# Optimization experiments

Hardware: AMD Instinct MI355X
Metric: run time of the kernel (lower is better)

The kernel has to match this reference:

```python
import jax, jax.numpy as jnp
import numpy as np

N = 100000   # total nodes
E = 500000   # directed edges
G = 100      # graphs in batch (1000 nodes each)
D = 146      # in/hidden/out dim
C = 10       # classes
BN_EPS = 1e-5


def setup_inputs():
    key = jax.random.key(0)
    ks = jax.random.split(key, 20)
    nodes_feat = jax.random.normal(ks[0], (N, D), jnp.float32)
    src = jax.random.randint(ks[1], (E,), 0, N, dtype=jnp.int32)
    dst = jax.random.randint(ks[2], (E,), 0, N, dtype=jnp.int32)
    graph_ids = (jnp.arange(N, dtype=jnp.int32) // (N // G)).astype(jnp.int32)
    snorm = jnp.full((N,), 1.0 / np.sqrt(N // G), jnp.float32)
    s = 0.05
    W_emb = jax.random.normal(ks[3], (D, D), jnp.float32) * s
    b_emb = jnp.zeros((D,), jnp.float32)
    Ws = jax.random.normal(ks[4], (4, D, D), jnp.float32) * s
    bs = jnp.zeros((4, D), jnp.float32)
    gammas = jnp.ones((4, D), jnp.float32)
    betas = jnp.zeros((4, D), jnp.float32)
    W1 = jax.random.normal(ks[5], (D, D // 2), jnp.float32) * s
    b1 = jnp.zeros((D // 2,), jnp.float32)
    W2 = jax.random.normal(ks[6], (D // 2, D // 4), jnp.float32) * s
    b2 = jnp.zeros((D // 4,), jnp.float32)
    W3 = jax.random.normal(ks[7], (D // 4, C), jnp.float32) * s
    b3 = jnp.zeros((C,), jnp.float32)
    return dict(nodes_feat=nodes_feat, snorm=snorm, W_emb=W_emb, b_emb=b_emb,
                Ws=Ws, bs=bs, gammas=gammas, betas=betas,
                W1=W1, b1=b1, W2=W2, b2=b2, W3=W3, b3=b3,
                src=src, dst=dst, graph_ids=graph_ids)


def _gcn_layer(h, W, b, gamma, beta, src, dst, norm_out, norm_in, snorm):
    h_in = h
    # GraphConv norm='both': D_out^{-1/2} on source, sum-aggregate, D_in^{-1/2} on dest
    m = (h * norm_out[:, None])[src]                     # [E, D] gather
    agg = jax.ops.segment_sum(m, dst, num_segments=N)    # [N, D] scatter-add
    h = agg * norm_in[:, None] @ W + b                   # linear
    h = h * snorm[:, None]                               # graph norm
    mu = jnp.mean(h, axis=0)
    var = jnp.var(h, axis=0)
    h = (h - mu) * jax.lax.rsqrt(var + BN_EPS) * gamma + beta  # batch norm
    h = jax.nn.relu(h)
    return h_in + h                                      # residual


def reference(nodes_feat, snorm, W_emb, b_emb, Ws, bs, gammas, betas,
              W1, b1, W2, b2, W3, b3, src, dst, graph_ids):
    ones_e = jnp.ones((E,), jnp.float32)
    deg_out = jnp.clip(jax.ops.segment_sum(ones_e, src, num_segments=N), 1.0)
    deg_in = jnp.clip(jax.ops.segment_sum(ones_e, dst, num_segments=N), 1.0)
    norm_out = jax.lax.rsqrt(deg_out)
    norm_in = jax.lax.rsqrt(deg_in)

    h = nodes_feat @ W_emb + b_emb                       # embedding_h
    for i in range(4):
        h = _gcn_layer(h, Ws[i], bs[i], gammas[i], betas[i],
                       src, dst, norm_out, norm_in, snorm)

    # mean_nodes per graph
    cnt = jax.ops.segment_sum(jnp.ones((N,), jnp.float32), graph_ids, num_segments=G)
    hg = jax.ops.segment_sum(h, graph_ids, num_segments=G) / cnt[:, None]

    # MLPReadout: 146 -> 73 -> 36 -> 10
    x = jax.nn.relu(hg @ W1 + b1)
    x = jax.nn.relu(x @ W2 + b2)
    return x @ W3 + b3
```

## Files before the change

kernel.cpp:

```cpp
#include <hip/hip_runtime.h>

#define N_NODES 100000
#define N_EDGES 500000
#define N_GRAPHS 100
#define DIM 146
#define APAD 160
#define HPAD 160
#define TPW 160
#define BN_EPS 1e-5f
#define GS_PART 8
#define GS_STRIDE 147
#define ST_PART 4

typedef __bf16 bf16x8 __attribute__((ext_vector_type(8)));
typedef float floatx4 __attribute__((ext_vector_type(4)));
typedef unsigned short ushort_t;
typedef unsigned int uint_t;

__device__ inline ushort_t f2bf(float x) {
  uint_t u = __float_as_uint(x);
  uint_t r = (u + 0x7fffu + ((u >> 16) & 1u)) >> 16;
  return (ushort_t)r;
}
__device__ inline float bf2f(ushort_t b) { return __uint_as_float((uint_t)b << 16); }
__device__ inline uint_t pack2bf(float a, float b) {
  return (uint_t)f2bf(a) | ((uint_t)f2bf(b) << 16);
}
__device__ inline float bflo(uint_t u) { return __uint_as_float(u << 16); }
__device__ inline float bfhi(uint_t u) { return __uint_as_float(u & 0xffff0000u); }

__device__ inline void async_cp16(const ushort_t* g, ushort_t* l) {
  __builtin_amdgcn_global_load_lds((const __attribute__((address_space(1))) void*)g,
                                   (__attribute__((address_space(3))) void*)l, 16, 0, 0);
}

__global__ void hist_kernel(const int* __restrict__ src, const int* __restrict__ dst,
                            int* __restrict__ deg_out, int* __restrict__ deg_in) {
  int e = blockIdx.x * 256 + threadIdx.x;
  if (e < N_EDGES) {
    atomicAdd(&deg_out[src[e]], 1);
    atomicAdd(&deg_in[dst[e]], 1);
  }
}

__global__ void norm_kernel(const int* __restrict__ deg_out, const int* __restrict__ deg_in,
                            float* __restrict__ norm_out, float* __restrict__ norm_in) {
  int v = blockIdx.x * 256 + threadIdx.x;
  if (v < N_NODES) {
    norm_out[v] = rsqrtf((float)max(deg_out[v], 1));
    norm_in[v]  = rsqrtf((float)max(deg_in[v], 1));
  }
}

__global__ void scan1_kernel(const int* __restrict__ deg_in, int* __restrict__ bsums) {
  __shared__ int sred[256];
  int t0 = blockIdx.x * 1024 + threadIdx.x * 4;
  int s = 0;
#pragma unroll
  for (int i = 0; i < 4; i++) { int v = t0 + i; s += (v < N_NODES) ? deg_in[v] : 0; }
  sred[threadIdx.x] = s; __syncthreads();
  for (int off = 128; off > 0; off >>= 1) {
    if (threadIdx.x < off) sred[threadIdx.x] += sred[threadIdx.x + off];
    __syncthreads();
  }
  if (threadIdx.x == 0) bsums[blockIdx.x] = sred[0];
}

__global__ void scan2_kernel(const int* __restrict__ bsums, int* __restrict__ bofs,
                             int* __restrict__ row_ptr, int nb) {
  if (threadIdx.x == 0 && blockIdx.x == 0) {
    int run = 0;
    for (int i = 0; i < nb; i++) { bofs[i] = run; run += bsums[i]; }
    row_ptr[N_NODES] = run;
  }
}

__global__ void scan3_kernel(const int* __restrict__ deg_in, const int* __restrict__ bofs,
                             int* __restrict__ row_ptr) {
  __shared__ int ssc[256];
  int t0 = blockIdx.x * 1024 + threadIdx.x * 4;
  int v4[4]; int s = 0;
#pragma unroll
  for (int i = 0; i < 4; i++) { int v = t0 + i; v4[i] = (v < N_NODES) ? deg_in[v] : 0; s += v4[i]; }
  ssc[threadIdx.x] = s; __syncthreads();
  for (int off = 1; off < 256; off <<= 1) {
    int t = (threadIdx.x >= off) ? ssc[threadIdx.x - off] : 0;
    __syncthreads();
    ssc[threadIdx.x] += t;
    __syncthreads();
  }
  int ex = ssc[threadIdx.x] - s + bofs[blockIdx.x];
#pragma unroll
  for (int i = 0; i < 4; i++) {
    int v = t0 + i;
    if (v < N_NODES) { row_ptr[v] = ex; ex += v4[i]; }
  }
}

__global__ void csr_fill_kernel(const int* __restrict__ src, const int* __restrict__ dst,
                                const int* __restrict__ row_ptr, int* __restrict__ fill,
                                int* __restrict__ csr) {
  int e = blockIdx.x * 256 + threadIdx.x;
  if (e < N_EDGES) {
    int d = dst[e];
    int slot = atomicAdd(&fill[d], 1);
    csr[row_ptr[d] + slot] = src[e];
  }
}

__global__ void wtrans_kernel(const float* __restrict__ W_emb, const float* __restrict__ Ws,
                              ushort_t* __restrict__ Wb, ushort_t* __restrict__ Wh) {
  int idx = blockIdx.x * 256 + threadIdx.x;
  if (idx >= 5 * 5 * 10 * 64 * 8) return;
  int j = idx & 7;
  int t = idx >> 3;
  int lane = t & 63; t >>= 6;
  int nt = t % 10; t /= 10;
  int kc = t % 5;
  int m = t / 5;
  const float* W = (m == 0) ? W_emb : Ws + (size_t)(m - 1) * DIM * DIM;
  int k = kc * 32 + (lane >> 4) * 8 + j;
  int n = nt * 16 + (lane & 15);
  float w = (k < DIM && n < DIM) ? W[k * DIM + n] : 0.f;
  ushort_t hi = f2bf(w);
  float lo = w - bf2f(hi);
  size_t base = (size_t)((((m * 5 + kc) * 10 + nt) * 2) * 64 + lane) * 8 + j;
  Wb[base] = hi;
  Wb[base + 512] = f2bf(lo);
  Wh[(size_t)(((m * 5 + kc) * 10 + nt) * 64 + lane) * 8 + j] = hi;
}

__device__ inline bf16x8 make_frag(const float* __restrict__ nf, int row, int kc, int quad) {
  union { bf16x8 v; ushort_t u[8]; } r;
  const float* p = nf + (size_t)row * DIM + kc * 32 + quad * 8;
  int c0 = kc * 32 + quad * 8;
  if (c0 + 8 <= DIM) {
    float2 q0 = *(const float2*)(p);
    float2 q1 = *(const float2*)(p + 2);
    float2 q2 = *(const float2*)(p + 4);
    float2 q3 = *(const float2*)(p + 6);
    r.u[0] = f2bf(q0.x); r.u[1] = f2bf(q0.y); r.u[2] = f2bf(q1.x); r.u[3] = f2bf(q1.y);
    r.u[4] = f2bf(q2.x); r.u[5] = f2bf(q2.y); r.u[6] = f2bf(q3.x); r.u[7] = f2bf(q3.y);
  } else {
#pragma unroll
    for (int j = 0; j < 8; j++) r.u[j] = (c0 + j < DIM) ? f2bf(p[j]) : (ushort_t)0;
  }
  return r.v;
}

__global__ __launch_bounds__(256, 3) void gemm_embed_kernel(
    const float* __restrict__ nf, const ushort_t* __restrict__ Wb,
    const float* __restrict__ bias, const float* __restrict__ norm_out,
    float* __restrict__ h, ushort_t* __restrict__ hb) {
  __shared__ __align__(16) ushort_t sB[2][10240];
  int wave = threadIdx.x >> 6, lane = threadIdx.x & 63;
  int quad = lane >> 4, l16 = lane & 15;
  int m0 = blockIdx.x * 128 + wave * 32;
  int ra = min(m0 + l16, N_NODES - 1);
  int rb = min(m0 + 16 + l16, N_NODES - 1);

  auto stage = [&](int buf, int kc) {
    const ushort_t* wsrc = Wb + (size_t)kc * 10240 + threadIdx.x * 8;
    ushort_t* ldst = &sB[buf][threadIdx.x * 8];
#pragma unroll
    for (int p = 0; p < 5; p++) async_cp16(wsrc + p * 2048, ldst + p * 2048);
  };

  stage(0, 0);
  __syncthreads();

  floatx4 acc[2][10];
#pragma unroll
  for (int s = 0; s < 2; s++)
#pragma unroll
    for (int nt = 0; nt < 10; nt++) acc[s][nt] = (floatx4){0.f, 0.f, 0.f, 0.f};

#pragma unroll
  for (int kc = 0; kc < 5; kc++) {
    int buf = kc & 1;
    if (kc < 4) stage(buf ^ 1, kc + 1);
    bf16x8 a0 = make_frag(nf, ra, kc, quad);
    bf16x8 a1 = make_frag(nf, rb, kc, quad);
    const ushort_t* bp = &sB[buf][lane * 8];
#pragma unroll
    for (int nt = 0; nt < 10; nt++) {
      bf16x8 bh = *(const bf16x8*)(bp + (nt * 2) * 512);
      bf16x8 bl = *(const bf16x8*)(bp + (nt * 2 + 1) * 512);
      acc[0][nt] = __builtin_amdgcn_mfma_f32_16x16x32_bf16(a0, bh, acc[0][nt], 0, 0, 0);
      acc[1][nt] = __builtin_amdgcn_mfma_f32_16x16x32_bf16(a1, bh, acc[1][nt], 0, 0, 0);
      acc[0][nt] = __builtin_amdgcn_mfma_f32_16x16x32_bf16(a0, bl, acc[0][nt], 0, 0, 0);
      acc[1][nt] = __builtin_amdgcn_mfma_f32_16x16x32_bf16(a1, bl, acc[1][nt], 0, 0, 0);
    }
    __syncthreads();
  }

  float no[2][4];
#pragma unroll
  for (int s = 0; s < 2; s++)
#pragma unroll
    for (int r = 0; r < 4; r++) no[s][r] = norm_out[min(m0 + s * 16 + quad * 4 + r, N_NODES - 1)];

  float* sF = (float*)&sB[0][0];
#pragma unroll
  for (int nt = 0; nt < 5; nt++) {
    int c = nt * 16 + l16;
    float b = bias[c];
#pragma unroll
    for (int s = 0; s < 2; s++)
#pragma unroll
      for (int r = 0; r < 4; r++)
        sF[(wave * 32 + s * 16 + quad * 4 + r) * 80 + c] = acc[s][nt][r] + b;
  }
  __syncthreads();
#pragma unroll
  for (int i = 0; i < 10; i++) {
    int n = threadIdx.x + i * 256;
    int row = n / 20, ch = n - row * 20;
    int grow = blockIdx.x * 128 + row;
    if (grow < N_NODES)
      *((uint4*)(h + (size_t)grow * HPAD) + ch) = ((const uint4*)(sF + row * 80))[ch];
  }
  __syncthreads();
#pragma unroll
  for (int nt = 5; nt < 10; nt++) {
    int c = nt * 16 + l16;
    float b = (c < DIM) ? bias[c] : 0.f;
#pragma unroll
    for (int s = 0; s < 2; s++)
#pragma unroll
      for (int r = 0; r < 4; r++)
        sF[(wave * 32 + s * 16 + quad * 4 + r) * 80 + (c - 80)] = acc[s][nt][r] + b;
  }
  __syncthreads();
#pragma unroll
  for (int i = 0; i < 10; i++) {
    int n = threadIdx.x + i * 256;
    int row = n / 20, ch = n - row * 20;
    int grow = blockIdx.x * 128 + row;
    if (grow < N_NODES)
      *((uint4*)(h + (size_t)grow * HPAD + 80) + ch) = ((const uint4*)(sF + row * 80))[ch];
  }
  __syncthreads();
  ushort_t* sC = &sB[0][0];
#pragma unroll
  for (int nt = 0; nt < 10; nt++) {
    int c = nt * 16 + l16;
    float b = (c < DIM) ? bias[c] : 0.f;
#pragma unroll
    for (int s = 0; s < 2; s++)
#pragma unroll
      for (int r = 0; r < 4; r++)
        sC[(wave * 32 + s * 16 + quad * 4 + r) * 160 + c] = f2bf((acc[s][nt][r] + b) * no[s][r]);
  }
  __syncthreads();
#pragma unroll
  for (int i = 0; i < 10; i++) {
    int n = threadIdx.x + i * 256;
    int row = n / 20, ch = n - row * 20;
    int grow = blockIdx.x * 128 + row;
    if (grow < N_NODES)
      *((uint4*)(hb + (size_t)grow * APAD) + ch) = ((const uint4*)(sC + row * 160))[ch];
  }
}

__global__ __launch_bounds__(256, 4) void gemm_kernel(
    const ushort_t* __restrict__ Abf, const ushort_t* __restrict__ Wh,
    const float* __restrict__ bias, const float* __restrict__ snorm,
    ushort_t* __restrict__ tmpb, float* __restrict__ stats) {
  __shared__ __align__(16) ushort_t sB[2][5120];
  __shared__ float sred[2 * DIM];
  int wave = threadIdx.x >> 6, lane = threadIdx.x & 63;
  int quad = lane >> 4, l16 = lane & 15;
  int m0 = blockIdx.x * 128 + wave * 32;
  int ra = min(m0 + l16, N_NODES - 1);
  int rb = min(m0 + 16 + l16, N_NODES - 1);
  const ushort_t* ap0 = Abf + (size_t)ra * APAD + quad * 8;
  const ushort_t* ap1 = Abf + (size_t)rb * APAD + quad * 8;

  auto stage = [&](int buf, int kc) {
    const ushort_t* wsrc = Wh + (size_t)kc * 5120;
    ushort_t* ldst = &sB[buf][0];
    async_cp16(wsrc + threadIdx.x * 8, ldst + threadIdx.x * 8);
    async_cp16(wsrc + (threadIdx.x + 256) * 8, ldst + (threadIdx.x + 256) * 8);
    if (threadIdx.x < 128)
      async_cp16(wsrc + (threadIdx.x + 512) * 8, ldst + (threadIdx.x + 512) * 8);
  };

  stage(0, 0);
  bf16x8 a0[5], a1[5];
#pragma unroll
  for (int kc = 0; kc < 5; kc++) {
    a0[kc] = *(const bf16x8*)(ap0 + kc * 32);
    a1[kc] = *(const bf16x8*)(ap1 + kc * 32);
  }
  for (int i = threadIdx.x; i < 2 * DIM; i += 256) sred[i] = 0.f;
  __syncthreads();

  floatx4 acc[2][10];
#pragma unroll
  for (int s = 0; s < 2; s++)
#pragma unroll
    for (int nt = 0; nt < 10; nt++) acc[s][nt] = (floatx4){0.f, 0.f, 0.f, 0.f};

  for (int kc = 0; kc < 5; kc++) {
    int buf = kc & 1;
    if (kc < 4) stage(buf ^ 1, kc + 1);
    const ushort_t* bp = &sB[buf][lane * 8];
#pragma unroll
    for (int nt = 0; nt < 10; nt++) {
      bf16x8 bh = *(const bf16x8*)(bp + nt * 512);
      acc[0][nt] = __builtin_amdgcn_mfma_f32_16x16x32_bf16(a0[kc], bh, acc[0][nt], 0, 0, 0);
      acc[1][nt] = __builtin_amdgcn_mfma_f32_16x16x32_bf16(a1[kc], bh, acc[1][nt], 0, 0, 0);
    }
    __syncthreads();
  }

  float sn[2][4];
#pragma unroll
  for (int s = 0; s < 2; s++)
#pragma unroll
    for (int r = 0; r < 4; r++) sn[s][r] = snorm[min(m0 + s * 16 + quad * 4 + r, N_NODES - 1)];
#pragma unroll
  for (int nt = 0; nt < 10; nt++) {
    int c = nt * 16 + l16;
    if (c < DIM) {
      float b = bias[c];
      float ssum = 0.f, ssq = 0.f;
#pragma unroll
      for (int s = 0; s < 2; s++)
#pragma unroll
        for (int r = 0; r < 4; r++) {
          if (m0 + s * 16 + quad * 4 + r < N_NODES) {
            float val = (acc[s][nt][r] + b) * sn[s][r];
            ssum += val; ssq += val * val;
          }
        }
      ssum += __shfl_xor(ssum, 16, 64); ssum += __shfl_xor(ssum, 32, 64);
      ssq  += __shfl_xor(ssq, 16, 64);  ssq  += __shfl_xor(ssq, 32, 64);
      if (quad == 0) {
        atomicAdd(&sred[c], ssum);
        atomicAdd(&sred[DIM + c], ssq);
      }
    }
  }

  ushort_t* sC = &sB[0][0];
#pragma unroll
  for (int half = 0; half < 2; half++) {
    __syncthreads();
    if ((wave >> 1) == half) {
      int lrow = (wave & 1) * 32;
#pragma unroll
      for (int nt = 0; nt < 10; nt++) {
        int c = nt * 16 + l16;
        float b = (c < DIM) ? bias[c] : 0.f;
#pragma unroll
        for (int s = 0; s < 2; s++)
#pragma unroll
          for (int r = 0; r < 4; r++)
            sC[(lrow + s * 16 + quad * 4 + r) * TPW + c] = f2bf((acc[s][nt][r] + b) * sn[s][r]);
      }
    }
    __syncthreads();
    uint4* gp = (uint4*)(tmpb + ((size_t)blockIdx.x * 128 + half * 64) * TPW);
#pragma unroll
    for (int i = 0; i < 5; i++) {
      int n = threadIdx.x + i * 256;
      gp[n] = *(const uint4*)(sC + n * 8);
    }
  }
  float* stp = stats + (blockIdx.x & (ST_PART - 1)) * 2 * DIM;
  for (int i = threadIdx.x; i < 2 * DIM; i += 256) atomicAdd(&stp[i], sred[i]);
}

__global__ __launch_bounds__(256) void agg_kernel(
    const ushort_t* __restrict__ hb, const int* __restrict__ row_ptr,
    const int* __restrict__ csr, const float* __restrict__ norm_in,
    ushort_t* __restrict__ xb) {
  int wid = threadIdx.x >> 6, lane = threadIdx.x & 63;
  int v = blockIdx.x * 4 + wid;
  if (v >= N_NODES) return;
  int e0 = row_ptr[v], e1 = row_ptr[v + 1];
  bool act = lane < 40;
  int col8 = lane * 4;
  float a0 = 0.f, a1 = 0.f, a2 = 0.f, a3 = 0.f;
  float b0 = 0.f, b1 = 0.f, b2 = 0.f, b3 = 0.f;
  int e = e0;
  for (; e + 1 < e1; e += 2) {
    int s0 = csr[e], s1 = csr[e + 1];
    if (act) {
      uint2 u0 = *(const uint2*)(hb + (size_t)s0 * APAD + col8);
      uint2 u1 = *(const uint2*)(hb + (size_t)s1 * APAD + col8);
      a0 += bflo(u0.x); a1 += bfhi(u0.x); a2 += bflo(u0.y); a3 += bfhi(u0.y);
      b0 += bflo(u1.x); b1 += bfhi(u1.x); b2 += bflo(u1.y); b3 += bfhi(u1.y);
    }
  }
  if (e < e1) {
    int s0 = csr[e];
    if (act) {
      uint2 u0 = *(const uint2*)(hb + (size_t)s0 * APAD + col8);
      a0 += bflo(u0.x); a1 += bfhi(u0.x); a2 += bflo(u0.y); a3 += bfhi(u0.y);
    }
  }
  if (act) {
    float ni = norm_in[v];
    uint2 o;
    o.x = pack2bf((a0 + b0) * ni, (a1 + b1) * ni);
    o.y = pack2bf((a2 + b2) * ni, (a3 + b3) * ni);
    *(uint2*)((uint_t*)(xb + (size_t)v * APAD) + lane * 2) = o;
  }
}

__global__ __launch_bounds__(256) void bn_kernel(const ushort_t* __restrict__ tmpb,
                                                 const float* __restrict__ stats,
                                                 const float* __restrict__ gamma,
                                                 const float* __restrict__ beta,
                                                 const float* __restrict__ norm_out,
                                                 float* __restrict__ h,
                                                 ushort_t* __restrict__ hb) {
  __shared__ float2 scs[DIM / 2], shs[DIM / 2];
  int t = threadIdx.x;
  if (t < DIM / 2) {
    int c0 = 2 * t, c1 = c0 + 1;
    float su0 = 0.f, su1 = 0.f, sq0 = 0.f, sq1 = 0.f;
#pragma unroll
    for (int p = 0; p < ST_PART; p++) {
      const float* sp = stats + p * 2 * DIM;
      su0 += sp[c0]; su1 += sp[c1];
      sq0 += sp[DIM + c0]; sq1 += sp[DIM + c1];
    }
    float mu0 = su0 * (1.f / N_NODES), mu1 = su1 * (1.f / N_NODES);
    float v0 = sq0 * (1.f / N_NODES) - mu0 * mu0;
    float v1 = sq1 * (1.f / N_NODES) - mu1 * mu1;
    float s0 = gamma[c0] * rsqrtf(v0 + BN_EPS), s1 = gamma[c1] * rsqrtf(v1 + BN_EPS);
    scs[t] = make_float2(s0, s1);
    shs[t] = make_float2(beta[c0] - mu0 * s0, beta[c1] - mu1 * s1);
  }
  __syncthreads();
  int idx = blockIdx.x * 256 + t;
  if (idx >= N_NODES * (DIM / 2)) return;
  int v = idx / (DIM / 2), c2 = idx - v * (DIM / 2);
  uint_t tu = ((const uint_t*)tmpb)[(size_t)v * (TPW / 2) + c2];
  float2 sc = scs[c2], sh = shs[c2];
  float2* hp = (float2*)(h + (size_t)v * HPAD + 2 * c2);
  float2 hv = *hp;
  float x0 = fmaf(bflo(tu), sc.x, sh.x); x0 = fmaxf(x0, 0.f);
  float x1 = fmaf(bfhi(tu), sc.y, sh.y); x1 = fmaxf(x1, 0.f);
  hv.x += x0; hv.y += x1;
  *hp = hv;
  float no = norm_out[v];
  ((uint_t*)hb)[(size_t)v * (APAD / 2) + c2] = pack2bf(hv.x * no, hv.y * no);
}

__global__ __launch_bounds__(192) void gsum_kernel(
    const ushort_t* __restrict__ tmpb, const float* __restrict__ stats,
    const float* __restrict__ gamma, const float* __restrict__ beta,
    const float* __restrict__ h, const int* __restrict__ gids,
    float* __restrict__ hgp) {
  int t = threadIdx.x;
  if (t > DIM) return;
  float sc = 0.f, sh = 0.f;
  if (t < DIM) {
    float su = 0.f, sq = 0.f;
#pragma unroll
    for (int p = 0; p < ST_PART; p++) {
      const float* sp = stats + p * 2 * DIM;
      su += sp[t]; sq += sp[DIM + t];
    }
    float mu = su * (1.f / N_NODES);
    float var = sq * (1.f / N_NODES) - mu * mu;
    sc = gamma[t] * rsqrtf(var + BN_EPS);
    sh = beta[t] - mu * sc;
  }
  int r0 = blockIdx.x * 64;
  int part = blockIdx.x & (GS_PART - 1);
  float accv = 0.f;
  int g_prev = gids[r0];
  for (int rr = 0; rr < 64; rr++) {
    int r = r0 + rr;
    if (r >= N_NODES) break;
    int g = gids[r];
    if (g != g_prev) {
      atomicAdd(&hgp[(size_t)(part * N_GRAPHS + g_prev) * GS_STRIDE + t], accv);
      accv = 0.f; g_prev = g;
    }
    float val;
    if (t < DIM) {
      float x = fmaf(bf2f(tmpb[(size_t)r * TPW + t]), sc, sh);
      x = fmaxf(x, 0.f);
      val = h[(size_t)r * HPAD + t] + x;
    } else {
      val = 1.f;
    }
    accv += val;
  }
  atomicAdd(&hgp[(size_t)(part * N_GRAPHS + g_prev) * GS_STRIDE + t], accv);
}

__global__ __launch_bounds__(256) void mlp_kernel(
    const float* __restrict__ hgp,
    const float* __restrict__ W1, const float* __restrict__ b1,
    const float* __restrict__ W2, const float* __restrict__ b2,
    const float* __restrict__ W3, const float* __restrict__ b3,
    float* __restrict__ out) {
  __shared__ float hrow[DIM];
  __shared__ float x1[73];
  __shared__ float x2[36];
  int g = blockIdx.x;
  int t = threadIdx.x;
  if (t < DIM) {
    float s = 0.f, cnt = 0.f;
#pragma unroll
    for (int p = 0; p < GS_PART; p++) {
      const float* row = hgp + (size_t)(p * N_GRAPHS + g) * GS_STRIDE;
      s += row[t];
      cnt += row[DIM];
    }
    hrow[t] = s / cnt;
  }
  __syncthreads();
  if (t < 73) {
    float s = b1[t];
    for (int k = 0; k < DIM; k++) s = fmaf(hrow[k], W1[k * 73 + t], s);
    x1[t] = s > 0.f ? s : 0.f;
  }
  __syncthreads();
  if (t < 36) {
    float s = b2[t];
    for (int k = 0; k < 73; k++) s = fmaf(x1[k], W2[k * 36 + t], s);
    x2[t] = s > 0.f ? s : 0.f;
  }
  __syncthreads();
  if (t < 10) {
    float s = b3[t];
    for (int k = 0; k < 36; k++) s = fmaf(x2[k], W3[k * 10 + t], s);
    out[g * 10 + t] = s;
  }
}

extern "C" void kernel_launch(void* const* d_in, const int* in_sizes, int n_in,
                              void* d_out, int out_size, void* d_ws, size_t ws_size,
                              hipStream_t stream) {
  const float* nodes_feat = (const float*)d_in[0];
  const float* snorm  = (const float*)d_in[1];
  const float* W_emb  = (const float*)d_in[2];
  const float* b_emb  = (const float*)d_in[3];
  const float* Ws     = (const float*)d_in[4];
  const float* bs     = (const float*)d_in[5];
  const float* gammas = (const float*)d_in[6];
  const float* betas  = (const float*)d_in[7];
  const float* W1 = (const float*)d_in[8];
  const float* b1 = (const float*)d_in[9];
  const float* W2 = (const float*)d_in[10];
  const float* b2 = (const float*)d_in[11];
  const float* W3 = (const float*)d_in[12];
  const float* b3 = (const float*)d_in[13];
  const int* src  = (const int*)d_in[14];
  const int* dst  = (const int*)d_in[15];
  const int* gids = (const int*)d_in[16];
  float* out = (float*)d_out;

  const int GB = (N_NODES + 127) / 128;
  const int NPADROWS = GB * 128;

  char* base = (char*)d_ws;
  size_t off = 0;
  auto alloc = [&](size_t bytes) { void* p = base + off; off += (bytes + 255) & ~size_t(255); return p; };
  float* h    = (float*)alloc((size_t)N_NODES * HPAD * 4);
  ushort_t* tmpb = (ushort_t*)alloc((size_t)NPADROWS * TPW * 2);
  ushort_t* xb = (ushort_t*)alloc((size_t)N_NODES * APAD * 2);
  ushort_t* hb = (ushort_t*)alloc((size_t)N_NODES * APAD * 2);
  char* zstart = base + off;
  int* deg_out = (int*)alloc(N_NODES * 4);
  int* deg_in  = (int*)alloc(N_NODES * 4);
  int* fill    = (int*)alloc(N_NODES * 4);
  float* stats = (float*)alloc(4 * ST_PART * 2 * DIM * 4);
  float* hgp   = (float*)alloc((size_t)GS_PART * N_GRAPHS * GS_STRIDE * 4);
  size_t zbytes = (size_t)((base + off) - zstart);
  int* row_ptr = (int*)alloc((N_NODES + 1) * 4);
  float* norm_out = (float*)alloc(N_NODES * 4);
  float* norm_in  = (float*)alloc(N_NODES * 4);
  int* csr   = (int*)alloc((size_t)N_EDGES * 4);
  int* bsums = (int*)alloc(128 * 4);
  int* bofs  = (int*)alloc(128 * 4);
  ushort_t* Wb = (ushort_t*)alloc((size_t)5 * 5 * 10 * 2 * 64 * 8 * 2);
  ushort_t* Wh = (ushort_t*)alloc((size_t)5 * 5 * 10 * 64 * 8 * 2);

  hipMemsetAsync(zstart, 0, zbytes, stream);

  hist_kernel<<<(N_EDGES + 255) / 256, 256, 0, stream>>>(src, dst, deg_out, deg_in);
  norm_kernel<<<(N_NODES + 255) / 256, 256, 0, stream>>>(deg_out, deg_in, norm_out, norm_in);
  int nb = (N_NODES + 1023) / 1024;
  scan1_kernel<<<nb, 256, 0, stream>>>(deg_in, bsums);
  scan2_kernel<<<1, 64, 0, stream>>>(bsums, bofs, row_ptr, nb);
  scan3_kernel<<<nb, 256, 0, stream>>>(deg_in, bofs, row_ptr);
  csr_fill_kernel<<<(N_EDGES + 255) / 256, 256, 0, stream>>>(src, dst, row_ptr, fill, csr);
  wtrans_kernel<<<(5 * 5 * 10 * 64 * 8 + 255) / 256, 256, 0, stream>>>(W_emb, Ws, Wb, Wh);

  const size_t WM = (size_t)5 * 10 * 2 * 64 * 8;
  const size_t WHM = (size_t)5 * 10 * 64 * 8;

  gemm_embed_kernel<<<GB, 256, 0, stream>>>(nodes_feat, Wb, b_emb, norm_out, h, hb);

  for (int l = 0; l < 4; l++) {
    float* st = stats + (size_t)l * ST_PART * 2 * DIM;
    agg_kernel<<<(N_NODES + 3) / 4, 256, 0, stream>>>(hb, row_ptr, csr, norm_in, xb);
    gemm_kernel<<<GB, 256, 0, stream>>>(xb, Wh + (size_t)(l + 1) * WHM, bs + l * DIM,
                                        snorm, tmpb, st);
    if (l < 3) {
      bn_kernel<<<(N_NODES * (DIM / 2) + 255) / 256, 256, 0, stream>>>(
          tmpb, st, gammas + l * DIM, betas + l * DIM, norm_out, h, hb);
    } else {
      gsum_kernel<<<(N_NODES + 63) / 64, 192, 0, stream>>>(
          tmpb, st, gammas + l * DIM, betas + l * DIM, h, gids, hgp);
    }
  }

  mlp_kernel<<<N_GRAPHS, 256, 0, stream>>>(hgp, W1, b1, W2, b2, W3, b3, out);
}
```

Measured before the change: 717.7 us.

## Fuse GEMM with batch-norm epilogue via in-kernel grid barrier

```diff
diff --git a/kernel.cpp b/kernel.cpp
--- a/kernel.cpp
+++ b/kernel.cpp
@@ -6,11 +6,11 @@
 #define DIM 146
 #define APAD 160
 #define HPAD 160
-#define TPW 160
 #define BN_EPS 1e-5f
 #define GS_PART 8
 #define GS_STRIDE 147
 #define ST_PART 4
+#define GRID_GB 782
 
 typedef __bf16 bf16x8 __attribute__((ext_vector_type(8)));
 typedef float floatx4 __attribute__((ext_vector_type(4)));
@@ -263,12 +263,18 @@
   }
 }
 
-__global__ __launch_bounds__(256, 4) void gemm_kernel(
+template <bool LAST>
+__global__ __launch_bounds__(256, 4) void gemm_bn_kernel(
     const ushort_t* __restrict__ Abf, const ushort_t* __restrict__ Wh,
     const float* __restrict__ bias, const float* __restrict__ snorm,
-    ushort_t* __restrict__ tmpb, float* __restrict__ stats) {
+    float* __restrict__ stats, const float* __restrict__ gamma,
+    const float* __restrict__ beta, const float* __restrict__ norm_out,
+    float* __restrict__ h, ushort_t* __restrict__ hb,
+    const int* __restrict__ gids, float* __restrict__ hgp, int* __restrict__ gbar) {
   __shared__ __align__(16) ushort_t sB[2][5120];
+  __shared__ __align__(16) ushort_t sHB[5120];
   __shared__ float sred[2 * DIM];
+  __shared__ float sbn[2 * DIM];
   int wave = threadIdx.x >> 6, lane = threadIdx.x & 63;
   int quad = lane >> 4, l16 = lane & 15;
   int m0 = blockIdx.x * 128 + wave * 32;
@@ -315,23 +321,33 @@
     __syncthreads();
   }
 
-  float sn[2][4];
+  float sn[2][4], no[2][4];
 #pragma unroll
   for (int s = 0; s < 2; s++)
 #pragma unroll
-    for (int r = 0; r < 4; r++) sn[s][r] = snorm[min(m0 + s * 16 + quad * 4 + r, N_NODES - 1)];
+    for (int r = 0; r < 4; r++) {
+      int row = min(m0 + s * 16 + quad * 4 + r, N_NODES - 1);
+      sn[s][r] = snorm[row];
+      no[s][r] = LAST ? 0.f : norm_out[row];
+    }
+  float bv[10];
+#pragma unroll
+  for (int nt = 0; nt < 10; nt++) {
+    int c = nt * 16 + l16;
+    bv[nt] = (c < DIM) ? bias[c] : 0.f;
+  }
+
 #pragma unroll
   for (int nt = 0; nt < 10; nt++) {
     int c = nt * 16 + l16;
     if (c < DIM) {
-      float b = bias[c];
       float ssum = 0.f, ssq = 0.f;
 #pragma unroll
       for (int s = 0; s < 2; s++)
 #pragma unroll
         for (int r = 0; r < 4; r++) {
           if (m0 + s * 16 + quad * 4 + r < N_NODES) {
-            float val = (acc[s][nt][r] + b) * sn[s][r];
+            float val = (acc[s][nt][r] + bv[nt]) * sn[s][r];
             ssum += val; ssq += val * val;
           }
         }
@@ -343,34 +359,103 @@
       }
     }
   }
-
-  ushort_t* sC = &sB[0][0];
-#pragma unroll
-  for (int half = 0; half < 2; half++) {
-    __syncthreads();
-    if ((wave >> 1) == half) {
-      int lrow = (wave & 1) * 32;
+  __syncthreads();
+  {
+    float* stp = stats + (blockIdx.x & (ST_PART - 1)) * 2 * DIM;
+    for (int i = threadIdx.x; i < 2 * DIM; i += 256) atomicAdd(&stp[i], sred[i]);
+  }
+
+  __syncthreads();
+  if (threadIdx.x == 0) {
+    __threadfence();
+    atomicAdd(gbar, 1);
+    while (__hip_atomic_load(gbar, __ATOMIC_ACQUIRE, __HIP_MEMORY_SCOPE_AGENT) < GRID_GB)
+      __builtin_amdgcn_s_sleep(8);
+  }
+  __syncthreads();
+
+  for (int c = threadIdx.x; c < DIM; c += 256) {
+    float su = 0.f, sq = 0.f;
+#pragma unroll
+    for (int p = 0; p < ST_PART; p++) {
+      su += __hip_atomic_load(&stats[p * 2 * DIM + c], __ATOMIC_RELAXED, __HIP_MEMORY_SCOPE_AGENT);
+      sq += __hip_atomic_load(&stats[p * 2 * DIM + DIM + c], __ATOMIC_RELAXED, __HIP_MEMORY_SCOPE_AGENT);
+    }
+    float mu = su * (1.f / N_NODES);
+    float var = sq * (1.f / N_NODES) - mu * mu;
+    float sc = gamma[c] * rsqrtf(var + BN_EPS);
+    sbn[c] = sc;
+    sbn[DIM + c] = beta[c] - mu * sc;
+  }
+  __syncthreads();
+
+  float* sH = (float*)&sB[0][0];
+  uint4* sH4 = (uint4*)sH;
+  for (int p = 0; p < 4; p++) {
+    int pr0 = blockIdx.x * 128 + p * 32;
+    const uint4* hg4 = (const uint4*)(h + (size_t)pr0 * HPAD);
+#pragma unroll
+    for (int i = 0; i < 5; i++) {
+      int n = threadIdx.x + i * 256;
+      sH4[n] = (pr0 + n / 40 < N_NODES) ? hg4[n] : make_uint4(0, 0, 0, 0);
+    }
+    __syncthreads();
+    if (wave == p) {
 #pragma unroll
       for (int nt = 0; nt < 10; nt++) {
         int c = nt * 16 + l16;
-        float b = (c < DIM) ? bias[c] : 0.f;
 #pragma unroll
         for (int s = 0; s < 2; s++)
 #pragma unroll
-          for (int r = 0; r < 4; r++)
-            sC[(lrow + s * 16 + quad * 4 + r) * TPW + c] = f2bf((acc[s][nt][r] + b) * sn[s][r]);
+          for (int r = 0; r < 4; r++) {
+            int gi = (s * 16 + quad * 4 + r) * 160 + c;
+            if (c < DIM) {
+              float val = (acc[s][nt][r] + bv[nt]) * sn[s][r];
+              float x = fmaxf(fmaf(val, sbn[c], sbn[DIM + c]), 0.f);
+              float hnew = sH[gi] + x;
+              sH[gi] = hnew;
+              if (!LAST) ((ushort_t*)sHB)[gi] = f2bf(hnew * no[s][r]);
+            } else {
+              if (!LAST) ((ushort_t*)sHB)[gi] = 0;
+            }
+          }
       }
     }
     __syncthreads();
-    uint4* gp = (uint4*)(tmpb + ((size_t)blockIdx.x * 128 + half * 64) * TPW);
-#pragma unroll
-    for (int i = 0; i < 5; i++) {
-      int n = threadIdx.x + i * 256;
-      gp[n] = *(const uint4*)(sC + n * 8);
-    }
-  }
-  float* stp = stats + (blockIdx.x & (ST_PART - 1)) * 2 * DIM;
-  for (int i = threadIdx.x; i < 2 * DIM; i += 256) atomicAdd(&stp[i], sred[i]);
+    if (!LAST) {
+      uint4* hw4 = (uint4*)(h + (size_t)pr0 * HPAD);
+#pragma unroll
+      for (int i = 0; i < 5; i++) {
+        int n = threadIdx.x + i * 256;
+        if (pr0 + n / 40 < N_NODES) hw4[n] = sH4[n];
+      }
+      uint4* hb4 = (uint4*)(hb + (size_t)pr0 * APAD);
+#pragma unroll
+      for (int i = 0; i < 3; i++) {
+        int n = threadIdx.x + i * 256;
+        if (n < 640 && pr0 + n / 20 < N_NODES) hb4[n] = ((const uint4*)sHB)[n];
+      }
+    } else {
+      int t = threadIdx.x;
+      if (t <= DIM && pr0 < N_NODES) {
+        int part = blockIdx.x & (GS_PART - 1);
+        float accv = 0.f;
+        int g_prev = gids[pr0];
+        for (int rr = 0; rr < 32; rr++) {
+          int r = pr0 + rr;
+          if (r >= N_NODES) break;
+          int g = gids[r];
+          if (g != g_prev) {
+            atomicAdd(&hgp[(size_t)(part * N_GRAPHS + g_prev) * GS_STRIDE + t], accv);
+            accv = 0.f; g_prev = g;
+          }
+          accv += (t < DIM) ? sH[rr * 160 + t] : 1.f;
+        }
+        atomicAdd(&hgp[(size_t)(part * N_GRAPHS + g_prev) * GS_STRIDE + t], accv);
+      }
+    }
+    __syncthreads();
+  }
 }
 
 __global__ __launch_bounds__(256) void agg_kernel(
@@ -409,92 +494,6 @@
     o.y = pack2bf((a2 + b2) * ni, (a3 + b3) * ni);
     *(uint2*)((uint_t*)(xb + (size_t)v * APAD) + lane * 2) = o;
   }
-}
-
-__global__ __launch_bounds__(256) void bn_kernel(const ushort_t* __restrict__ tmpb,
-                                                 const float* __restrict__ stats,
-                                                 const float* __restrict__ gamma,
-                                                 const float* __restrict__ beta,
-                                                 const float* __restrict__ norm_out,
-                                                 float* __restrict__ h,
-                                                 ushort_t* __restrict__ hb) {
-  __shared__ float2 scs[DIM / 2], shs[DIM / 2];
-  int t = threadIdx.x;
-  if (t < DIM / 2) {
-    int c0 = 2 * t, c1 = c0 + 1;
-    float su0 = 0.f, su1 = 0.f, sq0 = 0.f, sq1 = 0.f;
-#pragma unroll
-    for (int p = 0; p < ST_PART; p++) {
-      const float* sp = stats + p * 2 * DIM;
-      su0 += sp[c0]; su1 += sp[c1];
-      sq0 += sp[DIM + c0]; sq1 += sp[DIM + c1];
-    }
-    float mu0 = su0 * (1.f / N_NODES), mu1 = su1 * (1.f / N_NODES);
-    float v0 = sq0 * (1.f / N_NODES) - mu0 * mu0;
-    float v1 = sq1 * (1.f / N_NODES) - mu1 * mu1;
-    float s0 = gamma[c0] * rsqrtf(v0 + BN_EPS), s1 = gamma[c1] * rsqrtf(v1 + BN_EPS);
-    scs[t] = make_float2(s0, s1);
-    shs[t] = make_float2(beta[c0] - mu0 * s0, beta[c1] - mu1 * s1);
-  }
-  __syncthreads();
-  int idx = blockIdx.x * 256 + t;
-  if (idx >= N_NODES * (DIM / 2)) return;
-  int v = idx / (DIM / 2), c2 = idx - v * (DIM / 2);
-  uint_t tu = ((const uint_t*)tmpb)[(size_t)v * (TPW / 2) + c2];
-  float2 sc = scs[c2], sh = shs[c2];
-  float2* hp = (float2*)(h + (size_t)v * HPAD + 2 * c2);
-  float2 hv = *hp;
-  float x0 = fmaf(bflo(tu), sc.x, sh.x); x0 = fmaxf(x0, 0.f);
-  float x1 = fmaf(bfhi(tu), sc.y, sh.y); x1 = fmaxf(x1, 0.f);
-  hv.x += x0; hv.y += x1;
-  *hp = hv;
-  float no = norm_out[v];
-  ((uint_t*)hb)[(size_t)v * (APAD / 2) + c2] = pack2bf(hv.x * no, hv.y * no);
-}
-
-__global__ __launch_bounds__(192) void gsum_kernel(
-    const ushort_t* __restrict__ tmpb, const float* __restrict__ stats,
-    const float* __restrict__ gamma, const float* __restrict__ beta,
-    const float* __restrict__ h, const int* __restrict__ gids,
-    float* __restrict__ hgp) {
-  int t = threadIdx.x;
-  if (t > DIM) return;
-  float sc = 0.f, sh = 0.f;
-  if (t < DIM) {
-    float su = 0.f, sq = 0.f;
-#pragma unroll
-    for (int p = 0; p < ST_PART; p++) {
-      const float* sp = stats + p * 2 * DIM;
-      su += sp[t]; sq += sp[DIM + t];
-    }
-    float mu = su * (1.f / N_NODES);
-    float var = sq * (1.f / N_NODES) - mu * mu;
-    sc = gamma[t] * rsqrtf(var + BN_EPS);
-    sh = beta[t] - mu * sc;
-  }
-  int r0 = blockIdx.x * 64;
-  int part = blockIdx.x & (GS_PART - 1);
-  float accv = 0.f;
-  int g_prev = gids[r0];
-  for (int rr = 0; rr < 64; rr++) {
-    int r = r0 + rr;
-    if (r >= N_NODES) break;
-    int g = gids[r];
-    if (g != g_prev) {
-      atomicAdd(&hgp[(size_t)(part * N_GRAPHS + g_prev) * GS_STRIDE + t], accv);
-      accv = 0.f; g_prev = g;
-    }
-    float val;
-    if (t < DIM) {
-      float x = fmaf(bf2f(tmpb[(size_t)r * TPW + t]), sc, sh);
-      x = fmaxf(x, 0.f);
-      val = h[(size_t)r * HPAD + t] + x;
-    } else {
-      val = 1.f;
-    }
-    accv += val;
-  }
-  atomicAdd(&hgp[(size_t)(part * N_GRAPHS + g_prev) * GS_STRIDE + t], accv);
 }
 
 __global__ __launch_bounds__(256) void mlp_kernel(
@@ -560,14 +559,12 @@
   const int* gids = (const int*)d_in[16];
   float* out = (float*)d_out;
 
-  const int GB = (N_NODES + 127) / 128;
-  const int NPADROWS = GB * 128;
+  const int GB = GRID_GB;
 
   char* base = (char*)d_ws;
   size_t off = 0;
   auto alloc = [&](size_t bytes) { void* p = base + off; off += (bytes + 255) & ~size_t(255); return p; };
   float* h    = (float*)alloc((size_t)N_NODES * HPAD * 4);
-  ushort_t* tmpb = (ushort_t*)alloc((size_t)NPADROWS * TPW * 2);
   ushort_t* xb = (ushort_t*)alloc((size_t)N_NODES * APAD * 2);
   ushort_t* hb = (ushort_t*)alloc((size_t)N_NODES * APAD * 2);
   char* zstart = base + off;
@@ -576,6 +573,7 @@
   int* fill    = (int*)alloc(N_NODES * 4);
   float* stats = (float*)alloc(4 * ST_PART * 2 * DIM * 4);
   float* hgp   = (float*)alloc((size_t)GS_PART * N_GRAPHS * GS_STRIDE * 4);
+  int* gbar    = (int*)alloc(4 * 4);
   size_t zbytes = (size_t)((base + off) - zstart);
   int* row_ptr = (int*)alloc((N_NODES + 1) * 4);
   float* norm_out = (float*)alloc(N_NODES * 4);
@@ -597,7 +595,6 @@
   csr_fill_kernel<<<(N_EDGES + 255) / 256, 256, 0, stream>>>(src, dst, row_ptr, fill, csr);
   wtrans_kernel<<<(5 * 5 * 10 * 64 * 8 + 255) / 256, 256, 0, stream>>>(W_emb, Ws, Wb, Wh);
 
-  const size_t WM = (size_t)5 * 10 * 2 * 64 * 8;
   const size_t WHM = (size_t)5 * 10 * 64 * 8;
 
   gemm_embed_kernel<<<GB, 256, 0, stream>>>(nodes_feat, Wb, b_emb, norm_out, h, hb);
@@ -605,14 +602,14 @@
   for (int l = 0; l < 4; l++) {
     float* st = stats + (size_t)l * ST_PART * 2 * DIM;
     agg_kernel<<<(N_NODES + 3) / 4, 256, 0, stream>>>(hb, row_ptr, csr, norm_in, xb);
-    gemm_kernel<<<GB, 256, 0, stream>>>(xb, Wh + (size_t)(l + 1) * WHM, bs + l * DIM,
-                                        snorm, tmpb, st);
     if (l < 3) {
-      bn_kernel<<<(N_NODES * (DIM / 2) + 255) / 256, 256, 0, stream>>>(
-          tmpb, st, gammas + l * DIM, betas + l * DIM, norm_out, h, hb);
+      gemm_bn_kernel<false><<<GB, 256, 0, stream>>>(
+          xb, Wh + (size_t)(l + 1) * WHM, bs + l * DIM, snorm, st,
+          gammas + l * DIM, betas + l * DIM, norm_out, h, hb, nullptr, nullptr, gbar + l);
     } else {
-      gsum_kernel<<<(N_NODES + 63) / 64, 192, 0, stream>>>(
-          tmpb, st, gammas + l * DIM, betas + l * DIM, h, gids, hgp);
+      gemm_bn_kernel<true><<<GB, 256, 0, stream>>>(
+          xb, Wh + (size_t)(l + 1) * WHM, bs + l * DIM, snorm, st,
+          gammas + l * DIM, betas + l * DIM, norm_out, h, nullptr, gids, hgp, gbar + l);
     }
   }
 
```

Result: slower. 1.092 ms (+52.2%).
